# Kernel optimization log

Hardware: AMD Instinct MI355X
Metric: run time of the kernel (lower is better)

Reference implementation:

```python
import jax, jax.numpy as jnp
import numpy as np

EMBED_DIM = 1024
HEAD_SIZE = 64
SEQ_LEN = 2048
BATCH = 32

def setup_inputs() -> dict:
    key = jax.random.key(0)
    kx, kk, kq, kv = jax.random.split(key, 4)
    s = 1.0 / np.sqrt(EMBED_DIM)
    x = jax.random.normal(kx, (BATCH, SEQ_LEN, EMBED_DIM), dtype=jnp.float32)
    Wk = jax.random.normal(kk, (EMBED_DIM, HEAD_SIZE), dtype=jnp.float32) * s
    Wq = jax.random.normal(kq, (EMBED_DIM, HEAD_SIZE), dtype=jnp.float32) * s
    Wv = jax.random.normal(kv, (EMBED_DIM, HEAD_SIZE), dtype=jnp.float32) * s
    return {"x": x, "Wk": Wk, "Wq": Wq, "Wv": Wv}

def reference(x, Wk, Wq, Wv):
    # x: [B,T,C]; projections (no bias, per config.bias=False)
    k = jnp.einsum('btc,ch->bth', x, Wk)
    q = jnp.einsum('btc,ch->bth', x, Wq)
    v = jnp.einsum('btc,ch->bth', x, Wv)
    # NOTE: original computes k @ q^T (rows=k positions), scaled by embed_dim**-0.5
    scale = EMBED_DIM ** (-0.5)
    wei = jnp.einsum('bih,bjh->bij', k, q) * scale  # [B,T,T]
    T = x.shape[1]
    causal = jnp.tril(jnp.ones((T, T), dtype=bool))
    wei = jnp.where(causal, wei, -jnp.inf)
    wei = jax.nn.softmax(wei, axis=-1)
    # dropout: eval mode -> identity
    return jnp.einsum('bij,bjh->bih', wei, v)
```

## Files before the change

### kernel.cpp

```cpp
#include <hip/hip_runtime.h>
#include <hip/hip_bf16.h>

#define BATCH 32
#define SEQ   2048
#define EMB   1024
#define HS    64
#define BT    (BATCH*SEQ)

typedef short s16x4 __attribute__((ext_vector_type(4)));
typedef short s16x8 __attribute__((ext_vector_type(8)));
typedef float f32x4 __attribute__((ext_vector_type(4)));
using u16 = unsigned short;

static __device__ __forceinline__ short f2bf(float f) {
  __hip_bfloat16 h = __float2bfloat16(f);
  return *reinterpret_cast<short*>(&h);
}
static __device__ __forceinline__ void gl_lds16(const void* g, void* l) {
  __builtin_amdgcn_global_load_lds(
      (const __attribute__((address_space(1))) unsigned int*)g,
      (__attribute__((address_space(3))) unsigned int*)l, 16, 0, 0);
}

#define MFMA __builtin_amdgcn_mfma_f32_16x16x32_bf16

__global__ __launch_bounds__(256) void wconv_kernel(
    const float* __restrict__ Wk, const float* __restrict__ Wq,
    const float* __restrict__ Wv, short* __restrict__ Wt)
{
  const int n = blockIdx.x;
  const int w = n >> 6, h = n & 63;
  const float* Wp = (w == 0) ? Wk : (w == 1) ? Wq : Wv;
  const int k0 = threadIdx.x * 4;
  s16x4 p;
  #pragma unroll
  for (int e = 0; e < 4; ++e) p[e] = f2bf(Wp[(size_t)(k0 + e) * HS + h]);
  *(s16x4*)(Wt + (size_t)n * EMB + k0) = p;
}

__global__ __launch_bounds__(256, 4) void proj_kernel(
    const float* __restrict__ x, const short* __restrict__ Wt,
    short* __restrict__ kb, short* __restrict__ qb, short* __restrict__ vt)
{
  __shared__ __align__(16) u16 xs[64][72];
  const int tid  = threadIdx.x;
  const int row0 = blockIdx.x * 64;
  const int w  = tid >> 6, l = tid & 63;
  const int lr = l & 15, lg = l >> 4;

  f32x4 acc[4][3];
  #pragma unroll
  for (int m = 0; m < 4; ++m)
    #pragma unroll
    for (int n = 0; n < 3; ++n) acc[m][n] = f32x4{0.f, 0.f, 0.f, 0.f};

  for (int k0 = 0; k0 < EMB; k0 += 64) {
    s16x8 bw[2][3];
    #pragma unroll
    for (int kk = 0; kk < 2; ++kk)
      #pragma unroll
      for (int n = 0; n < 3; ++n)
        bw[kk][n] = *(const s16x8*)(Wt + (size_t)(w*48 + n*16 + lr) * EMB + k0 + kk*32 + lg*8);
    __syncthreads();
    #pragma unroll
    for (int i = 0; i < 4; ++i) {
      const int idx = i * 256 + tid;
      const int r = idx >> 4, c4 = idx & 15;
      float4 t = *(const float4*)(x + (size_t)(row0 + r) * EMB + k0 + c4 * 4);
      s16x4 p;
      p[0] = f2bf(t.x); p[1] = f2bf(t.y); p[2] = f2bf(t.z); p[3] = f2bf(t.w);
      *(s16x4*)&xs[r][c4 * 4] = p;
    }
    __syncthreads();
    #pragma unroll
    for (int kk = 0; kk < 2; ++kk) {
      s16x8 a[4];
      #pragma unroll
      for (int m = 0; m < 4; ++m)
        a[m] = *(const s16x8*)&xs[m*16 + lr][kk*32 + lg*8];
      #pragma unroll
      for (int m = 0; m < 4; ++m)
        #pragma unroll
        for (int n = 0; n < 3; ++n)
          acc[m][n] = MFMA(a[m], bw[kk][n], acc[m][n], 0, 0, 0);
    }
  }

  const int b  = row0 >> 11;
  const int t0 = row0 & 2047;
  #pragma unroll
  for (int m = 0; m < 4; ++m) {
    const int trow = m*16 + lg*4;
    #pragma unroll
    for (int n = 0; n < 3; ++n) {
      const int nbase = w*48 + n*16;
      const int wm = nbase >> 6;
      const int h  = (nbase + lr) & 63;
      if (wm == 2) {
        s16x4 p;
        #pragma unroll
        for (int r = 0; r < 4; ++r) p[r] = f2bf(acc[m][n][r]);
        *(s16x4*)(vt + ((size_t)(b*64 + h)) * SEQ + t0 + trow) = p;
      } else {
        short* dst = (wm == 0) ? kb : qb;
        #pragma unroll
        for (int r = 0; r < 4; ++r)
          dst[(size_t)(row0 + trow + r) * HS + h] = f2bf(acc[m][n][r]);
      }
    }
  }
}

__global__ __launch_bounds__(256, 3) void attn_kernel(
    const short* __restrict__ kb, const short* __restrict__ qb,
    const short* __restrict__ vt, float* __restrict__ out)
{
  __shared__ __align__(16) u16 q_s[2][4096];
  __shared__ __align__(16) u16 v_s[2][4096];
  __shared__ __align__(16) u16 P_lds[4][16][72];
  const int bid = blockIdx.x;
  const int wg  = (bid & 7) * 128 + (bid >> 3);
  const int b   = wg >> 5;
  const int it  = 31 - (wg & 31);
  const int tid = threadIdx.x;
  const int w   = tid >> 6;
  const int lr  = tid & 15;
  const int lg  = (tid & 63) >> 4;
  const int iw0 = it * 64 + w * 16;

  const short* qbb = qb + (size_t)b * SEQ * HS;
  const short* vtb = vt + (size_t)b * 64 * SEQ;

  const int srow0 = (0*256 + tid) >> 3, sc80 = tid & 7;
  const int srow1 = (256 + tid) >> 3;
  const int gcol0 = (sc80 * 8) ^ ((srow0 & 7) << 3);
  const int gcol1 = (sc80 * 8) ^ ((srow1 & 7) << 3);

#define STAGE(BUF, J0) do {                                                    \
    u16* lq0 = &q_s[BUF][(w*64) * 8];                                          \
    u16* lv0 = &v_s[BUF][(w*64) * 8];                                          \
    u16* lq1 = &q_s[BUF][(256 + w*64) * 8];                                    \
    u16* lv1 = &v_s[BUF][(256 + w*64) * 8];                                    \
    gl_lds16(qbb + (size_t)((J0) + srow0) * HS + gcol0, lq0);                  \
    gl_lds16(vtb + (size_t)srow0 * SEQ + (J0) + gcol0, lv0);                   \
    gl_lds16(qbb + (size_t)((J0) + srow1) * HS + gcol1, lq1);                  \
    gl_lds16(vtb + (size_t)srow1 * SEQ + (J0) + gcol1, lv1);                   \
  } while (0)

  s16x8 ones;
  #pragma unroll
  for (int e = 0; e < 8; ++e) ones[e] = (short)0x3F80;

  s16x8 kfrag[2];
  {
    const short* kp = kb + ((size_t)(b*SEQ) + iw0 + lr) * HS + lg*8;
    kfrag[0] = *(const s16x8*)(kp);
    kfrag[1] = *(const s16x8*)(kp + 32);
  }

  f32x4 o[4];
  #pragma unroll
  for (int n = 0; n < 4; ++n) o[n] = f32x4{0.f, 0.f, 0.f, 0.f};
  f32x4 lac = f32x4{0.f, 0.f, 0.f, 0.f};

  STAGE(0, 0);
  __syncthreads();

  int cur = 0;
  #pragma unroll 1
  for (int jt = 0; jt <= it; ++jt) {
    if (jt < it) STAGE(cur ^ 1, (jt + 1) * 64);
    const u16* qsb = q_s[cur];
    const u16* vsb = v_s[cur];
    f32x4 sc[4];
    #pragma unroll
    for (int s = 0; s < 4; ++s) {
      const int row = s*16 + lr, base = row * 64, swz = (row & 7) << 3;
      s16x8 q0 = *(const s16x8*)&qsb[base + ((lg*8) ^ swz)];
      s16x8 q1 = *(const s16x8*)&qsb[base + ((32 + lg*8) ^ swz)];
      f32x4 z = f32x4{0.f, 0.f, 0.f, 0.f};
      z = MFMA(q0, kfrag[0], z, 0, 0, 0);
      z = MFMA(q1, kfrag[1], z, 0, 0, 0);
      sc[s] = z;
    }
    const bool diag = (jt == it);
    #pragma unroll
    for (int s = 0; s < 4; ++s) {
      s16x4 pk;
      #pragma unroll
      for (int r = 0; r < 4; ++r) {
        float e = __expf(fmaf(sc[s][r], 0.03125f, -4.0f));
        if (diag && (s*16 + lg*4 + r > w*16 + lr)) e = 0.f;
        pk[r] = f2bf(e);
      }
      *(s16x4*)&P_lds[w][lr][16*s + 4*lg] = pk;
    }
    s16x8 pA0 = *(const s16x8*)&P_lds[w][lr][8*lg];
    s16x8 pA1 = *(const s16x8*)&P_lds[w][lr][32 + 8*lg];
    __builtin_amdgcn_s_setprio(1);
    #pragma unroll
    for (int n = 0; n < 4; ++n) {
      const int rowh = n*16 + lr, base = rowh * 64, swz = (rowh & 7) << 3;
      s16x8 v0 = *(const s16x8*)&vsb[base + ((lg*8) ^ swz)];
      s16x8 v1 = *(const s16x8*)&vsb[base + ((32 + lg*8) ^ swz)];
      o[n] = MFMA(pA0, v0, o[n], 0, 0, 0);
      o[n] = MFMA(pA1, v1, o[n], 0, 0, 0);
    }
    lac = MFMA(pA0, ones, lac, 0, 0, 0);
    lac = MFMA(pA1, ones, lac, 0, 0, 0);
    __builtin_amdgcn_s_setprio(0);
    __syncthreads();
    cur ^= 1;
  }
#undef STAGE

  float inv[4];
  #pragma unroll
  for (int r = 0; r < 4; ++r) inv[r] = 1.f / lac[r];
  #pragma unroll
  for (int n = 0; n < 4; ++n)
    #pragma unroll
    for (int r = 0; r < 4; ++r)
      out[((size_t)(b*SEQ) + iw0 + lg*4 + r) * HS + n*16 + lr] = o[n][r] * inv[r];
}

extern "C" void kernel_launch(void* const* d_in, const int* in_sizes, int n_in,
                              void* d_out, int out_size, void* d_ws, size_t ws_size,
                              hipStream_t stream) {
  const float* x  = (const float*)d_in[0];
  const float* Wk = (const float*)d_in[1];
  const float* Wq = (const float*)d_in[2];
  const float* Wv = (const float*)d_in[3];
  float* out = (float*)d_out;
  const size_t PLANE = (size_t)BT * HS;
  short* kb = (short*)d_ws;
  short* qb = kb + PLANE;
  short* vt = kb + 2*PLANE;
  short* Wt = kb + 3*PLANE;

  wconv_kernel<<<192, 256, 0, stream>>>(Wk, Wq, Wv, Wt);
  proj_kernel<<<BT/64, 256, 0, stream>>>(x, Wt, kb, qb, vt);
  attn_kernel<<<BATCH*(SEQ/64), 256, 0, stream>>>(kb, qb, vt, out);
}
```

Before: 129.3 us.

## Double-buffer x tiles via direct global-to-LDS loads in projection kernel

The projection kernel now stages fp32 x tiles straight into LDS with global_load_lds into two buffers, prefetching the next K-slice while the MFMAs run on the current one. The bf16 conversion moves from the staging step to the point where A fragments are read from LDS, and an XOR swizzle is used to avoid bank conflicts. This removes one barrier per iteration and the register round trip for x. In exchange LDS use doubles and grows fourfold per buffer because tiles are stored as fp32, which may reduce occupancy, and the conversion work moves onto the MFMA critical path.

```diff
diff --git a/kernel.cpp b/kernel.cpp
--- a/kernel.cpp
+++ b/kernel.cpp
@@ -42,18 +42,33 @@
     const float* __restrict__ x, const short* __restrict__ Wt,
     short* __restrict__ kb, short* __restrict__ qb, short* __restrict__ vt)
 {
-  __shared__ __align__(16) u16 xs[64][72];
+  __shared__ __align__(16) float xsf[2][64*64];
   const int tid  = threadIdx.x;
   const int row0 = blockIdx.x * 64;
   const int w  = tid >> 6, l = tid & 63;
   const int lr = l & 15, lg = l >> 4;
 
+#define STAGEX(BUF, K0) do {                                                   \
+    _Pragma("unroll") for (int i = 0; i < 4; ++i) {                            \
+      const int slot = i*256 + tid;                                            \
+      const int srow = slot >> 4, sch = slot & 15;                             \
+      const int gch  = sch ^ ((srow & 7) << 1);                                \
+      gl_lds16(x + (size_t)(row0 + srow) * EMB + (K0) + gch*4,                 \
+               &xsf[BUF][(i*256 + w*64) * 4]);                                 \
+    }                                                                          \
+  } while (0)
+
   f32x4 acc[4][3];
   #pragma unroll
   for (int m = 0; m < 4; ++m)
     #pragma unroll
     for (int n = 0; n < 3; ++n) acc[m][n] = f32x4{0.f, 0.f, 0.f, 0.f};
 
+  STAGEX(0, 0);
+  __syncthreads();
+
+  int cur = 0;
+  #pragma unroll 1
   for (int k0 = 0; k0 < EMB; k0 += 64) {
     s16x8 bw[2][3];
     #pragma unroll
@@ -61,30 +76,32 @@
       #pragma unroll
       for (int n = 0; n < 3; ++n)
         bw[kk][n] = *(const s16x8*)(Wt + (size_t)(w*48 + n*16 + lr) * EMB + k0 + kk*32 + lg*8);
-    __syncthreads();
-    #pragma unroll
-    for (int i = 0; i < 4; ++i) {
-      const int idx = i * 256 + tid;
-      const int r = idx >> 4, c4 = idx & 15;
-      float4 t = *(const float4*)(x + (size_t)(row0 + r) * EMB + k0 + c4 * 4);
-      s16x4 p;
-      p[0] = f2bf(t.x); p[1] = f2bf(t.y); p[2] = f2bf(t.z); p[3] = f2bf(t.w);
-      *(s16x4*)&xs[r][c4 * 4] = p;
-    }
-    __syncthreads();
+    if (k0 + 64 < EMB) STAGEX(cur ^ 1, k0 + 64);
     #pragma unroll
     for (int kk = 0; kk < 2; ++kk) {
       s16x8 a[4];
       #pragma unroll
-      for (int m = 0; m < 4; ++m)
-        a[m] = *(const s16x8*)&xs[m*16 + lr][kk*32 + lg*8];
+      for (int m = 0; m < 4; ++m) {
+        const int row = m*16 + lr;
+        const int p0  = (kk*8 + lg*2) ^ ((row & 7) << 1);
+        const float* xp = &xsf[cur][row*64 + p0*4];
+        f32x4 xa = *(const f32x4*)xp;
+        f32x4 xb = *(const f32x4*)(xp + 4);
+        s16x8 av;
+        av[0]=f2bf(xa[0]); av[1]=f2bf(xa[1]); av[2]=f2bf(xa[2]); av[3]=f2bf(xa[3]);
+        av[4]=f2bf(xb[0]); av[5]=f2bf(xb[1]); av[6]=f2bf(xb[2]); av[7]=f2bf(xb[3]);
+        a[m] = av;
+      }
       #pragma unroll
       for (int m = 0; m < 4; ++m)
         #pragma unroll
         for (int n = 0; n < 3; ++n)
           acc[m][n] = MFMA(a[m], bw[kk][n], acc[m][n], 0, 0, 0);
     }
-  }
+    __syncthreads();
+    cur ^= 1;
+  }
+#undef STAGEX
 
   const int b  = row0 >> 11;
   const int t0 = row0 & 2047;
```

Result: no change. 131.4 us (+1.7%).

## Warp-specialize projection kernel with producer wave and double-buffered x tiles

Applied to the files above, without the earlier changes.

The projection kernel now dedicates wave 3 as a producer that loads and converts the next x tile to bf16 into a second LDS buffer. Waves 0-2 each compute one full 64-column projection (K, Q or V) from the current buffer. This replaces the two barriers per k-step with one and overlaps global loads with MFMA work. In exchange, a quarter of the waves do no matrix math and the compute waves carry more accumulators, which raises register pressure.

```diff
diff --git a/kernel.cpp b/kernel.cpp
--- a/kernel.cpp
+++ b/kernel.cpp
@@ -42,70 +42,85 @@
     const float* __restrict__ x, const short* __restrict__ Wt,
     short* __restrict__ kb, short* __restrict__ qb, short* __restrict__ vt)
 {
-  __shared__ __align__(16) u16 xs[64][72];
+  __shared__ __align__(16) u16 xs[2][64][72];
   const int tid  = threadIdx.x;
   const int row0 = blockIdx.x * 64;
   const int w  = tid >> 6, l = tid & 63;
   const int lr = l & 15, lg = l >> 4;
 
-  f32x4 acc[4][3];
+#define STAGEP(BUF, K0) do {                                                   \
+    _Pragma("unroll") for (int i = 0; i < 8; ++i) {                            \
+      const int slot = i*64 + l;                                               \
+      const int row = slot >> 3, c8 = slot & 7;                                \
+      const float* src = x + (size_t)(row0 + row) * EMB + (K0) + c8*8;         \
+      float4 ta = *(const float4*)src;                                         \
+      float4 tb = *(const float4*)(src + 4);                                   \
+      s16x8 p;                                                                 \
+      p[0]=f2bf(ta.x); p[1]=f2bf(ta.y); p[2]=f2bf(ta.z); p[3]=f2bf(ta.w);      \
+      p[4]=f2bf(tb.x); p[5]=f2bf(tb.y); p[6]=f2bf(tb.z); p[7]=f2bf(tb.w);      \
+      *(s16x8*)&xs[BUF][row][c8*8] = p;                                        \
+    }                                                                          \
+  } while (0)
+
+  f32x4 acc[4][4];
   #pragma unroll
   for (int m = 0; m < 4; ++m)
     #pragma unroll
-    for (int n = 0; n < 3; ++n) acc[m][n] = f32x4{0.f, 0.f, 0.f, 0.f};
-
+    for (int n = 0; n < 4; ++n) acc[m][n] = f32x4{0.f, 0.f, 0.f, 0.f};
+
+  if (w == 3) STAGEP(0, 0);
+  __syncthreads();
+
+  int cur = 0;
+  #pragma unroll 1
   for (int k0 = 0; k0 < EMB; k0 += 64) {
-    s16x8 bw[2][3];
-    #pragma unroll
-    for (int kk = 0; kk < 2; ++kk)
-      #pragma unroll
-      for (int n = 0; n < 3; ++n)
-        bw[kk][n] = *(const s16x8*)(Wt + (size_t)(w*48 + n*16 + lr) * EMB + k0 + kk*32 + lg*8);
+    if (w == 3) {
+      if (k0 + 64 < EMB) STAGEP(cur ^ 1, k0 + 64);
+    } else {
+      s16x8 bw[2][4];
+      #pragma unroll
+      for (int kk = 0; kk < 2; ++kk)
+        #pragma unroll
+        for (int n = 0; n < 4; ++n)
+          bw[kk][n] = *(const s16x8*)(Wt + (size_t)(w*64 + n*16 + lr) * EMB + k0 + kk*32 + lg*8);
+      #pragma unroll
+      for (int kk = 0; kk < 2; ++kk) {
+        s16x8 a[4];
+        #pragma unroll
+        for (int m = 0; m < 4; ++m)
+          a[m] = *(const s16x8*)&xs[cur][m*16 + lr][kk*32 + lg*8];
+        #pragma unroll
+        for (int m = 0; m < 4; ++m)
+          #pragma unroll
+          for (int n = 0; n < 4; ++n)
+            acc[m][n] = MFMA(a[m], bw[kk][n], acc[m][n], 0, 0, 0);
+      }
+    }
     __syncthreads();
-    #pragma unroll
-    for (int i = 0; i < 4; ++i) {
-      const int idx = i * 256 + tid;
-      const int r = idx >> 4, c4 = idx & 15;
-      float4 t = *(const float4*)(x + (size_t)(row0 + r) * EMB + k0 + c4 * 4);
-      s16x4 p;
-      p[0] = f2bf(t.x); p[1] = f2bf(t.y); p[2] = f2bf(t.z); p[3] = f2bf(t.w);
-      *(s16x4*)&xs[r][c4 * 4] = p;
-    }
-    __syncthreads();
-    #pragma unroll
-    for (int kk = 0; kk < 2; ++kk) {
-      s16x8 a[4];
-      #pragma unroll
-      for (int m = 0; m < 4; ++m)
-        a[m] = *(const s16x8*)&xs[m*16 + lr][kk*32 + lg*8];
-      #pragma unroll
-      for (int m = 0; m < 4; ++m)
-        #pragma unroll
-        for (int n = 0; n < 3; ++n)
-          acc[m][n] = MFMA(a[m], bw[kk][n], acc[m][n], 0, 0, 0);
-    }
-  }
-
-  const int b  = row0 >> 11;
-  const int t0 = row0 & 2047;
-  #pragma unroll
-  for (int m = 0; m < 4; ++m) {
-    const int trow = m*16 + lg*4;
-    #pragma unroll
-    for (int n = 0; n < 3; ++n) {
-      const int nbase = w*48 + n*16;
-      const int wm = nbase >> 6;
-      const int h  = (nbase + lr) & 63;
-      if (wm == 2) {
-        s16x4 p;
-        #pragma unroll
-        for (int r = 0; r < 4; ++r) p[r] = f2bf(acc[m][n][r]);
-        *(s16x4*)(vt + ((size_t)(b*64 + h)) * SEQ + t0 + trow) = p;
-      } else {
-        short* dst = (wm == 0) ? kb : qb;
-        #pragma unroll
-        for (int r = 0; r < 4; ++r)
-          dst[(size_t)(row0 + trow + r) * HS + h] = f2bf(acc[m][n][r]);
+    cur ^= 1;
+  }
+#undef STAGEP
+
+  if (w < 3) {
+    const int b  = row0 >> 11;
+    const int t0 = row0 & 2047;
+    #pragma unroll
+    for (int m = 0; m < 4; ++m) {
+      const int trow = m*16 + lg*4;
+      #pragma unroll
+      for (int n = 0; n < 4; ++n) {
+        const int h = n*16 + lr;
+        if (w == 2) {
+          s16x4 p;
+          #pragma unroll
+          for (int r = 0; r < 4; ++r) p[r] = f2bf(acc[m][n][r]);
+          *(s16x4*)(vt + ((size_t)(b*64 + h)) * SEQ + t0 + trow) = p;
+        } else {
+          short* dst = (w == 0) ? kb : qb;
+          #pragma unroll
+          for (int r = 0; r < 4; ++r)
+            dst[(size_t)(row0 + trow + r) * HS + h] = f2bf(acc[m][n][r]);
+        }
       }
     }
   }
```

Result: slower. 158.1 us (+22.3%).

## Restructure projection GEMM to per-wave row tiles without block barriers

Applied to the files above, without the earlier changes.

Each wave now owns 16 rows of x and computes all 192 output columns (K, Q and V) itself. It stages its own bf16-converted x fragment through a private LDS slice, so the two __syncthreads per k-step go away. The next x chunk is register-prefetched, and the step size drops to 32. The cost is that every wave reloads the full Wt slice from global/L2 each step, and the loop now runs twice as many steps with a single MFMA per weight fragment.

```diff
diff --git a/kernel.cpp b/kernel.cpp
--- a/kernel.cpp
+++ b/kernel.cpp
@@ -42,71 +42,57 @@
     const float* __restrict__ x, const short* __restrict__ Wt,
     short* __restrict__ kb, short* __restrict__ qb, short* __restrict__ vt)
 {
-  __shared__ __align__(16) u16 xs[64][72];
-  const int tid  = threadIdx.x;
+  __shared__ __align__(16) u16 xw[4][16][40];
+  const int tid = threadIdx.x;
   const int row0 = blockIdx.x * 64;
   const int w  = tid >> 6, l = tid & 63;
   const int lr = l & 15, lg = l >> 4;
-
-  f32x4 acc[4][3];
-  #pragma unroll
-  for (int m = 0; m < 4; ++m)
-    #pragma unroll
-    for (int n = 0; n < 3; ++n) acc[m][n] = f32x4{0.f, 0.f, 0.f, 0.f};
-
-  for (int k0 = 0; k0 < EMB; k0 += 64) {
-    s16x8 bw[2][3];
-    #pragma unroll
-    for (int kk = 0; kk < 2; ++kk)
-      #pragma unroll
-      for (int n = 0; n < 3; ++n)
-        bw[kk][n] = *(const s16x8*)(Wt + (size_t)(w*48 + n*16 + lr) * EMB + k0 + kk*32 + lg*8);
-    __syncthreads();
-    #pragma unroll
-    for (int i = 0; i < 4; ++i) {
-      const int idx = i * 256 + tid;
-      const int r = idx >> 4, c4 = idx & 15;
-      float4 t = *(const float4*)(x + (size_t)(row0 + r) * EMB + k0 + c4 * 4);
-      s16x4 p;
-      p[0] = f2bf(t.x); p[1] = f2bf(t.y); p[2] = f2bf(t.z); p[3] = f2bf(t.w);
-      *(s16x4*)&xs[r][c4 * 4] = p;
-    }
-    __syncthreads();
-    #pragma unroll
-    for (int kk = 0; kk < 2; ++kk) {
-      s16x8 a[4];
-      #pragma unroll
-      for (int m = 0; m < 4; ++m)
-        a[m] = *(const s16x8*)&xs[m*16 + lr][kk*32 + lg*8];
-      #pragma unroll
-      for (int m = 0; m < 4; ++m)
-        #pragma unroll
-        for (int n = 0; n < 3; ++n)
-          acc[m][n] = MFMA(a[m], bw[kk][n], acc[m][n], 0, 0, 0);
+  const int srow = l >> 2, scol = (l & 3) * 8;
+
+  const float* xbase = x + (size_t)(row0 + w*16 + srow) * EMB + scol;
+
+  f32x4 acc[12];
+  #pragma unroll
+  for (int n = 0; n < 12; ++n) acc[n] = f32x4{0.f, 0.f, 0.f, 0.f};
+
+  float4 xa = *(const float4*)(xbase);
+  float4 xb = *(const float4*)(xbase + 4);
+
+  #pragma unroll 1
+  for (int k0 = 0; k0 < EMB; k0 += 32) {
+    s16x8 p;
+    p[0]=f2bf(xa.x); p[1]=f2bf(xa.y); p[2]=f2bf(xa.z); p[3]=f2bf(xa.w);
+    p[4]=f2bf(xb.x); p[5]=f2bf(xb.y); p[6]=f2bf(xb.z); p[7]=f2bf(xb.w);
+    *(s16x8*)&xw[w][srow][scol] = p;
+    if (k0 + 32 < EMB) {
+      xa = *(const float4*)(xbase + k0 + 32);
+      xb = *(const float4*)(xbase + k0 + 36);
+    }
+    s16x8 a = *(const s16x8*)&xw[w][lr][lg*8];
+    #pragma unroll
+    for (int n = 0; n < 12; ++n) {
+      s16x8 bw = *(const s16x8*)(Wt + (size_t)(n*16 + lr) * EMB + k0 + lg*8);
+      acc[n] = MFMA(a, bw, acc[n], 0, 0, 0);
     }
   }
 
   const int b  = row0 >> 11;
   const int t0 = row0 & 2047;
-  #pragma unroll
-  for (int m = 0; m < 4; ++m) {
-    const int trow = m*16 + lg*4;
-    #pragma unroll
-    for (int n = 0; n < 3; ++n) {
-      const int nbase = w*48 + n*16;
-      const int wm = nbase >> 6;
-      const int h  = (nbase + lr) & 63;
-      if (wm == 2) {
-        s16x4 p;
-        #pragma unroll
-        for (int r = 0; r < 4; ++r) p[r] = f2bf(acc[m][n][r]);
-        *(s16x4*)(vt + ((size_t)(b*64 + h)) * SEQ + t0 + trow) = p;
-      } else {
-        short* dst = (wm == 0) ? kb : qb;
-        #pragma unroll
-        for (int r = 0; r < 4; ++r)
-          dst[(size_t)(row0 + trow + r) * HS + h] = f2bf(acc[m][n][r]);
-      }
+  const int trow = w*16 + lg*4;
+  #pragma unroll
+  for (int n = 0; n < 12; ++n) {
+    const int wm = n >> 2;
+    const int h  = (n*16 + lr) & 63;
+    if (wm == 2) {
+      s16x4 pk;
+      #pragma unroll
+      for (int r = 0; r < 4; ++r) pk[r] = f2bf(acc[n][r]);
+      *(s16x4*)(vt + ((size_t)(b*64 + h)) * SEQ + t0 + trow) = pk;
+    } else {
+      short* dst = (wm == 0) ? kb : qb;
+      #pragma unroll
+      for (int r = 0; r < 4; ++r)
+        dst[(size_t)(row0 + trow + r) * HS + h] = f2bf(acc[n][r]);
     }
   }
 }
```

Result: slower. 259.8 us (+100.9%).
